# Performance work log

Hardware: AMD Instinct MI355X
Metric: run time of the kernel (lower is better)

Reference implementation:

```python
import jax, jax.numpy as jnp
import numpy as np

N_NODES = 50000
N_EDGES = 800000
IN_FEAT = 128
NUM_CLASSES = 40


def _glorot(key, shape):
    fan_in, fan_out = shape
    lim = jnp.sqrt(6.0 / (fan_in + fan_out))
    return jax.random.uniform(key, shape, jnp.float32, -lim, lim)


def setup_inputs() -> dict:
    key = jax.random.key(0)
    ks = jax.random.split(key, 16)
    inp = {
        "x": jax.random.normal(ks[0], (N_NODES, IN_FEAT), jnp.float32),
        "edge_index": jax.random.randint(ks[1], (2, N_EDGES), 0, N_NODES, jnp.int64),
        "edge_weight": jax.random.uniform(ks[2], (N_EDGES,), jnp.float32),
        # GCNConv weights (PyG GCNConv: linear w/o bias, separate bias added after aggregation)
        "W1": _glorot(ks[3], (IN_FEAT, 512)), "b1": jnp.zeros((512,), jnp.float32),
        "W2": _glorot(ks[4], (512, 256)), "b2": jnp.zeros((256,), jnp.float32),
        "W3": _glorot(ks[5], (256, 128)), "b3": jnp.zeros((128,), jnp.float32),
        # MLP head
        "L1w": _glorot(ks[6], (128, 64)), "L1b": jnp.zeros((64,), jnp.float32),
        "L2w": _glorot(ks[7], (64, 32)), "L2b": jnp.zeros((32,), jnp.float32),
        "L3w": _glorot(ks[8], (32, NUM_CLASSES)), "L3b": jnp.zeros((NUM_CLASSES,), jnp.float32),
    }
    return inp


def _gcn_conv(x, W, b, src, dst, ew, n):
    # PyG GCNConv: add self-loops (weight 1), symmetric normalization D^-1/2 (A+I) D^-1/2,
    # linear transform first, then scatter-add aggregation, then bias.
    xw = x @ W  # [N, C_out]
    deg = jax.ops.segment_sum(ew, dst, num_segments=n) + 1.0  # +1 for self-loop weight
    dinv = jnp.where(deg > 0, jax.lax.rsqrt(deg), 0.0)  # [N]
    norm = dinv[src] * ew * dinv[dst]  # [E]
    out = jax.ops.segment_sum(norm[:, None] * xw[src], dst, num_segments=n)
    out = out + (dinv * dinv)[:, None] * xw  # self-loop contribution
    return out + b


def reference(x, edge_index, edge_weight, W1, b1, W2, b2, W3, b3,
              L1w, L1b, L2w, L2b, L3w, L3b):
    n = x.shape[0]
    src, dst = edge_index[0], edge_index[1]
    # conv stack; dropout p=0.0 -> identity (omitted)
    h = jax.nn.relu(_gcn_conv(x, W1, b1, src, dst, edge_weight, n))
    h = jax.nn.relu(_gcn_conv(h, W2, b2, src, dst, edge_weight, n))
    h = jax.nn.relu(_gcn_conv(h, W3, b3, src, dst, edge_weight, n))
    # MLP head
    h = jax.nn.relu(h @ L1w + L1b)
    h = jax.nn.relu(h @ L2w + L2b)
    h = h @ L3w + L3b
    return jax.nn.softmax(h, axis=1)
```

## Files before the change

### kernel.cpp

```cpp
#include <hip/hip_runtime.h>
#include <hip/hip_bf16.h>

#define N_NODES 50000
#define N_EDGES 800000
#define M_PAD 50048

typedef __attribute__((ext_vector_type(8))) short short8;
typedef __attribute__((ext_vector_type(4))) float float4_;

#define GLOAD_LDS(g, l) __builtin_amdgcn_global_load_lds( \
    (const __attribute__((address_space(1))) void*)(g),   \
    (__attribute__((address_space(3))) void*)(l), 16, 0, 0)

__device__ __forceinline__ unsigned short f2bf(float f) {
    unsigned int u = __float_as_uint(f);
    unsigned int r = (u + 0x7FFFu + ((u >> 16) & 1u)) >> 16;
    return (unsigned short)r;
}
__device__ __forceinline__ float bf2f(unsigned short h) {
    return __uint_as_float(((unsigned int)h) << 16);
}


__global__ __launch_bounds__(256) void deg_kernel(const int* __restrict__ dst,
                                                  const float* __restrict__ ew,
                                                  float* __restrict__ deg, int E) {
    int e = blockIdx.x * blockDim.x + threadIdx.x;
    if (e < E) atomicAdd(&deg[dst[e]], ew[e]);
}

__global__ __launch_bounds__(256) void dinv_kernel(float* __restrict__ deg, int n) {
    int i = blockIdx.x * blockDim.x + threadIdx.x;
    if (i < n) deg[i] = rsqrtf(deg[i] + 1.0f);
}


__global__ __launch_bounds__(256) void count_kernel(const int* __restrict__ dst,
                                                    int* __restrict__ cnt, int E) {
    int e = blockIdx.x * blockDim.x + threadIdx.x;
    if (e < E) atomicAdd(&cnt[dst[e]], 1);
}

__global__ __launch_bounds__(512) void scan_block_kernel(const int* __restrict__ cnt,
                                                         int* __restrict__ rowptr,
                                                         int* __restrict__ bsums, int n) {
    __shared__ int s[512];
    int t = threadIdx.x;
    int i = blockIdx.x * 512 + t;
    s[t] = (i < n) ? cnt[i] : 0;
    __syncthreads();
    for (int off = 1; off < 512; off <<= 1) {
        int v = (t >= off) ? s[t - off] : 0;
        __syncthreads();
        s[t] += v;
        __syncthreads();
    }
    if (i < n) rowptr[i + 1] = s[t];
    if (t == 511) bsums[blockIdx.x] = s[511];
}

__global__ void scan_sums_kernel(int* bsums, int nb) {
    if (threadIdx.x == 0 && blockIdx.x == 0) {
        int run = 0;
        for (int i = 0; i < nb; ++i) { int v = bsums[i]; bsums[i] = run; run += v; }
    }
}

__global__ __launch_bounds__(512) void scan_add_kernel(int* __restrict__ rowptr,
                                                       const int* __restrict__ bsums, int n) {
    int i = blockIdx.x * 512 + threadIdx.x;
    if (i < n) rowptr[i + 1] += bsums[blockIdx.x];
    if (i == 0) rowptr[0] = 0;
}

__global__ __launch_bounds__(256) void fill_kernel(const int* __restrict__ src,
                                                   const int* __restrict__ dst,
                                                   const float* __restrict__ ew,
                                                   const float* __restrict__ dinv,
                                                   int* __restrict__ cursor,
                                                   int* __restrict__ col,
                                                   float* __restrict__ val, int E) {
    int e = blockIdx.x * blockDim.x + threadIdx.x;
    if (e >= E) return;
    int d = dst[e];
    int s = src[e];
    int pos = atomicAdd(&cursor[d], 1);
    col[pos] = s;
    val[pos] = dinv[s] * ew[e];
}


__global__ __launch_bounds__(256) void wsplit_kernel(const float* __restrict__ Wm,
                                                     unsigned short* __restrict__ Th,
                                                     unsigned short* __restrict__ Tl,
                                                     int K, int N) {
    int idx = blockIdx.x * blockDim.x + threadIdx.x;
    if (idx >= K * N) return;
    int n = idx / K, k = idx - n * K;
    float v = Wm[(size_t)k * N + n];
    unsigned short hi = f2bf(v);
    float res = v - bf2f(hi);
    Th[idx] = hi;
    Tl[idx] = f2bf(res);
}


template <int C, bool BIAS, bool RELU, bool SPLIT>
__global__ __launch_bounds__(256) void gather_kernel(const float* __restrict__ t,
                                                     const int* __restrict__ rowptr,
                                                     const int* __restrict__ col,
                                                     const float* __restrict__ val,
                                                     const float* __restrict__ dinv,
                                                     const float* __restrict__ bias,
                                                     float* __restrict__ outf,
                                                     unsigned short* __restrict__ oh,
                                                     unsigned short* __restrict__ ol, int n) {
    constexpr int R = C / 64;
    int wave = threadIdx.x >> 6, lane = threadIdx.x & 63;
    for (int node = blockIdx.x * 4 + wave; node < n; node += gridDim.x * 4) {
        float acc[R];
#pragma unroll
        for (int r = 0; r < R; ++r) acc[r] = 0.f;
        int p0 = rowptr[node], p1 = rowptr[node + 1];
        for (int p = p0; p < p1; ++p) {
            int s = col[p];
            float a = val[p];
            const float* tr = t + (size_t)s * C;
#pragma unroll
            for (int r = 0; r < R; ++r) acc[r] += a * tr[r * 64 + lane];
        }
        float di = dinv[node];
        const float* tn = t + (size_t)node * C;
#pragma unroll
        for (int r = 0; r < R; ++r) {
            float v = di * acc[r] + di * di * tn[r * 64 + lane];
            if (BIAS) v += bias[r * 64 + lane];
            if (RELU) v = fmaxf(v, 0.f);
            size_t idx = (size_t)node * C + r * 64 + lane;
            if (SPLIT) {
                unsigned short hi = f2bf(v);
                float res = v - bf2f(hi);
                oh[idx] = hi;
                ol[idx] = f2bf(res);
            } else {
                outf[idx] = v;
            }
        }
    }
}


template <int OUTMODE>
__global__ __launch_bounds__(256, 2) void mfma_gemm(const unsigned short* __restrict__ Ah,
                                                    const unsigned short* __restrict__ Al,
                                                    const unsigned short* __restrict__ Bh,
                                                    const unsigned short* __restrict__ Bl,
                                                    const float* __restrict__ bias,
                                                    float* __restrict__ Cf,
                                                    unsigned short* __restrict__ Ch,
                                                    unsigned short* __restrict__ Cl,
                                                    int K, int N) {
    __shared__ unsigned short sAh[128 * 64];
    __shared__ unsigned short sAl[128 * 64];
    __shared__ unsigned short sBh[128 * 64];
    __shared__ unsigned short sBl[128 * 64];

    int tid = threadIdx.x;
    int lane = tid & 63, w = tid >> 6;
    int m0 = blockIdx.x * 128, n0 = blockIdx.y * 128;

    const unsigned short* gsrc = (w == 0) ? Ah : (w == 1) ? Al : (w == 2) ? Bh : Bl;
    unsigned short* sbase = (w == 0) ? sAh : (w == 1) ? sAl : (w == 2) ? sBh : sBl;
    int grow0 = ((w < 2) ? m0 : n0) + (lane >> 3);
    int gcol = ((lane & 7) ^ ((lane >> 3) & 7)) * 8;
    const unsigned short* gptr0 = gsrc + (size_t)grow0 * K + gcol;

    float4_ acc[4][4] = {};

    int wm = (w >> 1) * 64, wn = (w & 1) * 64;
    int lr = lane & 15, lg = lane >> 4;

    for (int k0 = 0; k0 < K; k0 += 64) {
        const unsigned short* gp = gptr0 + k0;
#pragma unroll
        for (int q = 0; q < 16; ++q)
            GLOAD_LDS(gp + (size_t)(8 * q) * K, sbase + q * 512);
        __syncthreads();

#pragma unroll
        for (int ks = 0; ks < 2; ++ks) {
            short8 ahf[4], alf[4], bhf[4], blf[4];
#pragma unroll
            for (int f = 0; f < 4; ++f) {
                int ra = wm + f * 16 + lr;
                int sa = (((ks << 2) | lg) ^ (ra & 7)) * 16;
                ahf[f] = *(const short8*)((const char*)sAh + ra * 128 + sa);
                alf[f] = *(const short8*)((const char*)sAl + ra * 128 + sa);
                int rb = wn + f * 16 + lr;
                int sb = (((ks << 2) | lg) ^ (rb & 7)) * 16;
                bhf[f] = *(const short8*)((const char*)sBh + rb * 128 + sb);
                blf[f] = *(const short8*)((const char*)sBl + rb * 128 + sb);
            }
#pragma unroll
            for (int i = 0; i < 4; ++i)
#pragma unroll
                for (int j = 0; j < 4; ++j) {
                    acc[i][j] = __builtin_amdgcn_mfma_f32_16x16x32_bf16(ahf[i], bhf[j], acc[i][j], 0, 0, 0);
                    acc[i][j] = __builtin_amdgcn_mfma_f32_16x16x32_bf16(ahf[i], blf[j], acc[i][j], 0, 0, 0);
                    acc[i][j] = __builtin_amdgcn_mfma_f32_16x16x32_bf16(alf[i], bhf[j], acc[i][j], 0, 0, 0);
                }
        }
        __syncthreads();
    }

#pragma unroll
    for (int i = 0; i < 4; ++i) {
        int row0 = m0 + wm + i * 16 + lg * 4;
#pragma unroll
        for (int j = 0; j < 4; ++j) {
            int colg = n0 + wn + j * 16 + lr;
            float b = (OUTMODE == 1) ? bias[colg] : 0.f;
#pragma unroll
            for (int r = 0; r < 4; ++r) {
                float v = acc[i][j][r] + b;
                size_t idx = (size_t)(row0 + r) * N + colg;
                if (OUTMODE == 1) {
                    v = fmaxf(v, 0.f);
                    unsigned short hi = f2bf(v);
                    float res = v - bf2f(hi);
                    Ch[idx] = hi;
                    Cl[idx] = f2bf(res);
                } else {
                    Cf[idx] = v;
                }
            }
        }
    }
}


__global__ __launch_bounds__(256) void mlp_kernel(const float* __restrict__ h,
                                                  const float* __restrict__ W1, const float* __restrict__ b1,
                                                  const float* __restrict__ W2, const float* __restrict__ b2,
                                                  const float* __restrict__ W3, const float* __restrict__ b3,
                                                  float* __restrict__ out, int n) {
    __shared__ float W1s[128 * 64];
    __shared__ float W2s[64 * 32];
    __shared__ float W3s[32 * 40];
    __shared__ float b1s[64], b2s[32], b3s[40];
    __shared__ float hs[4][128];
    __shared__ float h1s[4][64];
    __shared__ float h2s[4][32];
    __shared__ float ls[4][40];
    __shared__ float es[4][40];

    int tid = threadIdx.x;
    for (int i = tid; i < 128 * 64; i += 256) W1s[i] = W1[i];
    for (int i = tid; i < 64 * 32; i += 256) W2s[i] = W2[i];
    for (int i = tid; i < 32 * 40; i += 256) W3s[i] = W3[i];
    if (tid < 64) b1s[tid] = b1[tid];
    if (tid < 32) b2s[tid] = b2[tid];
    if (tid < 40) b3s[tid] = b3[tid];
    __syncthreads();

    int wave = tid >> 6, lane = tid & 63;

    for (int base = blockIdx.x * 4; base < n; base += gridDim.x * 4) {
        int node = base + wave;
        if (node < n) {
            hs[wave][lane]      = fmaxf(h[(size_t)node * 128 + lane], 0.f);
            hs[wave][lane + 64] = fmaxf(h[(size_t)node * 128 + lane + 64], 0.f);
        }
        __syncthreads();
        {
            float acc = b1s[lane];
#pragma unroll 8
            for (int k = 0; k < 128; ++k) acc += hs[wave][k] * W1s[k * 64 + lane];
            h1s[wave][lane] = fmaxf(acc, 0.f);
        }
        __syncthreads();
        if (lane < 32) {
            float acc = b2s[lane];
#pragma unroll 8
            for (int k = 0; k < 64; ++k) acc += h1s[wave][k] * W2s[k * 32 + lane];
            h2s[wave][lane] = fmaxf(acc, 0.f);
        }
        __syncthreads();
        if (lane < 40) {
            float acc = b3s[lane];
#pragma unroll 8
            for (int k = 0; k < 32; ++k) acc += h2s[wave][k] * W3s[k * 40 + lane];
            ls[wave][lane] = acc;
        }
        __syncthreads();
        float e = 0.f;
        if (lane < 40) {
            float m = -1e30f;
            for (int j = 0; j < 40; ++j) m = fmaxf(m, ls[wave][j]);
            e = expf(ls[wave][lane] - m);
            es[wave][lane] = e;
        }
        __syncthreads();
        if (node < n && lane < 40) {
            float s = 0.f;
            for (int j = 0; j < 40; ++j) s += es[wave][j];
            out[(size_t)node * 40 + lane] = e / s;
        }
        __syncthreads();
    }
}


extern "C" void kernel_launch(void* const* d_in, const int* in_sizes, int n_in,
                              void* d_out, int out_size, void* d_ws, size_t ws_size,
                              hipStream_t stream) {
    const float* x   = (const float*)d_in[0];
    const int*   ei  = (const int*)d_in[1];
    const float* ew  = (const float*)d_in[2];
    const float* W1  = (const float*)d_in[3];
    const float* b1  = (const float*)d_in[4];
    const float* W2  = (const float*)d_in[5];
    const float* b2  = (const float*)d_in[6];
    const float* W3  = (const float*)d_in[7];
    const float* b3  = (const float*)d_in[8];
    const float* L1w = (const float*)d_in[9];
    const float* L1b = (const float*)d_in[10];
    const float* L2w = (const float*)d_in[11];
    const float* L2b = (const float*)d_in[12];
    const float* L3w = (const float*)d_in[13];
    const float* L3b = (const float*)d_in[14];
    float* out = (float*)d_out;

    const int n = N_NODES, E = N_EDGES;
    const int* src = ei;
    const int* dst = ei + E;

    char* wsb = (char*)d_ws;
    size_t off = 0;
    auto alloc = [&](size_t bytes) -> char* {
        char* p = wsb + off;
        off += (bytes + 255) & ~(size_t)255;
        return p;
    };
    float* dinv   = (float*)alloc(N_NODES * 4);
    int* rowptr   = (int*)alloc((N_NODES + 1) * 4);
    int* cursor   = (int*)alloc(N_NODES * 4);
    int* colb     = (int*)alloc((size_t)N_EDGES * 4);
    float* val    = (float*)alloc((size_t)N_EDGES * 4);
    int* bsums    = (int*)alloc(256 * 4);
    unsigned short* W1th = (unsigned short*)alloc(512 * 128 * 2);
    unsigned short* W1tl = (unsigned short*)alloc(512 * 128 * 2);
    unsigned short* W2th = (unsigned short*)alloc(256 * 512 * 2);
    unsigned short* W2tl = (unsigned short*)alloc(256 * 512 * 2);
    unsigned short* W3th = (unsigned short*)alloc(128 * 256 * 2);
    unsigned short* W3tl = (unsigned short*)alloc(128 * 256 * 2);
    unsigned short* aggXh = (unsigned short*)alloc((size_t)M_PAD * 128 * 2);
    unsigned short* aggXl = (unsigned short*)alloc((size_t)M_PAD * 128 * 2);
    unsigned short* h1h  = (unsigned short*)alloc((size_t)M_PAD * 512 * 2);
    unsigned short* h1l  = (unsigned short*)alloc((size_t)M_PAD * 512 * 2);
    float* t2     = (float*)alloc((size_t)M_PAD * 256 * 4);
    unsigned short* agg2h = aggXh;
    unsigned short* agg2l = (unsigned short*)h1h;
    float* t3   = (float*)((char*)h1h + (size_t)M_PAD * 256 * 2);
    float* agg3 = (float*)h1l;

    const int nb = (n + 511) / 512;

    hipMemsetAsync(dinv, 0, n * sizeof(float), stream);
    deg_kernel<<<(E + 255) / 256, 256, 0, stream>>>(dst, ew, dinv, E);
    dinv_kernel<<<(n + 255) / 256, 256, 0, stream>>>(dinv, n);

    wsplit_kernel<<<(128 * 512 + 255) / 256, 256, 0, stream>>>(W1, W1th, W1tl, 128, 512);
    wsplit_kernel<<<(512 * 256 + 255) / 256, 256, 0, stream>>>(W2, W2th, W2tl, 512, 256);
    wsplit_kernel<<<(256 * 128 + 255) / 256, 256, 0, stream>>>(W3, W3th, W3tl, 256, 128);

    hipMemsetAsync(cursor, 0, n * sizeof(int), stream);
    count_kernel<<<(E + 255) / 256, 256, 0, stream>>>(dst, cursor, E);
    scan_block_kernel<<<nb, 512, 0, stream>>>(cursor, rowptr, bsums, n);
    scan_sums_kernel<<<1, 64, 0, stream>>>(bsums, nb);
    scan_add_kernel<<<nb, 512, 0, stream>>>(rowptr, bsums, n);
    hipMemcpyAsync(cursor, rowptr, n * sizeof(int), hipMemcpyDeviceToDevice, stream);
    fill_kernel<<<(E + 255) / 256, 256, 0, stream>>>(src, dst, ew, dinv, cursor, colb, val, E);

    gather_kernel<128, false, false, true><<<(n + 3) / 4, 256, 0, stream>>>(
        x, rowptr, colb, val, dinv, nullptr, nullptr, aggXh, aggXl, n);
    {
        dim3 g(M_PAD / 128, 512 / 128);
        mfma_gemm<1><<<g, 256, 0, stream>>>(aggXh, aggXl, W1th, W1tl, b1, nullptr, h1h, h1l, 128, 512);
    }
    {
        dim3 g(M_PAD / 128, 256 / 128);
        mfma_gemm<0><<<g, 256, 0, stream>>>(h1h, h1l, W2th, W2tl, nullptr, t2, nullptr, nullptr, 512, 256);
    }
    gather_kernel<256, true, true, true><<<(n + 3) / 4, 256, 0, stream>>>(
        t2, rowptr, colb, val, dinv, b2, nullptr, agg2h, agg2l, n);
    {
        dim3 g(M_PAD / 128, 128 / 128);
        mfma_gemm<0><<<g, 256, 0, stream>>>(agg2h, agg2l, W3th, W3tl, nullptr, t3, nullptr, nullptr, 256, 128);
    }
    gather_kernel<128, true, false, false><<<(n + 3) / 4, 256, 0, stream>>>(
        t3, rowptr, colb, val, dinv, b3, agg3, nullptr, nullptr, n);
    mlp_kernel<<<1024, 256, 0, stream>>>(agg3, L1w, L1b, L2w, L2b, L3w, L3b, out, n);
}
```

Baseline: 761.9 us.

## Vectorize SpMM gather with float4 loads and unrolled multi-edge batching

Reworks the CSR gather kernel so each lane handles four contiguous features through float4 loads. When C is 128 the wave splits into two edge slots that are reduced with a cross-lane shuffle. Edges are processed four at a time per slot, with clamped index loads, so several independent row fetches are in flight to hide gather latency. Epilogue stores are vectorized as float4 or ushort4. The cost is extra masked loads on the tail and, for C=128, half the lanes sit idle during the epilogue.

```diff
diff --git a/kernel.cpp b/kernel.cpp
--- a/kernel.cpp
+++ b/kernel.cpp
@@ -115,35 +115,75 @@
                                                      float* __restrict__ outf,
                                                      unsigned short* __restrict__ oh,
                                                      unsigned short* __restrict__ ol, int n) {
-    constexpr int R = C / 64;
+    constexpr int L = C / 4;
+    constexpr int EPS = 64 / L;
+    constexpr int U = 4;
     int wave = threadIdx.x >> 6, lane = threadIdx.x & 63;
+    int slot = lane / L, li = lane % L;
+
     for (int node = blockIdx.x * 4 + wave; node < n; node += gridDim.x * 4) {
-        float acc[R];
-#pragma unroll
-        for (int r = 0; r < R; ++r) acc[r] = 0.f;
         int p0 = rowptr[node], p1 = rowptr[node + 1];
-        for (int p = p0; p < p1; ++p) {
-            int s = col[p];
-            float a = val[p];
-            const float* tr = t + (size_t)s * C;
-#pragma unroll
-            for (int r = 0; r < R; ++r) acc[r] += a * tr[r * 64 + lane];
-        }
-        float di = dinv[node];
-        const float* tn = t + (size_t)node * C;
-#pragma unroll
-        for (int r = 0; r < R; ++r) {
-            float v = di * acc[r] + di * di * tn[r * 64 + lane];
-            if (BIAS) v += bias[r * 64 + lane];
-            if (RELU) v = fmaxf(v, 0.f);
-            size_t idx = (size_t)node * C + r * 64 + lane;
+        float4 acc = {0.f, 0.f, 0.f, 0.f};
+        for (int pb = p0; pb < p1; pb += U * EPS) {
+            float a[U];
+            float4 v[U];
+#pragma unroll
+            for (int u = 0; u < U; ++u) {
+                int pe = pb + u * EPS + slot;
+                int pec = min(pe, p1 - 1);
+                int s = col[pec];
+                float av = val[pec];
+                a[u] = (pe < p1) ? av : 0.f;
+                v[u] = *(const float4*)(t + (size_t)s * C + li * 4);
+            }
+#pragma unroll
+            for (int u = 0; u < U; ++u) {
+                acc.x += a[u] * v[u].x;
+                acc.y += a[u] * v[u].y;
+                acc.z += a[u] * v[u].z;
+                acc.w += a[u] * v[u].w;
+            }
+        }
+        if (EPS == 2) {
+            acc.x += __shfl_xor(acc.x, 32);
+            acc.y += __shfl_xor(acc.y, 32);
+            acc.z += __shfl_xor(acc.z, 32);
+            acc.w += __shfl_xor(acc.w, 32);
+        }
+        if (EPS == 1 || slot == 0) {
+            float di = dinv[node];
+            float s2 = di * di;
+            float4 tv = *(const float4*)(t + (size_t)node * C + li * 4);
+            float4 r;
+            r.x = di * acc.x + s2 * tv.x;
+            r.y = di * acc.y + s2 * tv.y;
+            r.z = di * acc.z + s2 * tv.z;
+            r.w = di * acc.w + s2 * tv.w;
+            if (BIAS) {
+                float4 b4 = *(const float4*)(bias + li * 4);
+                r.x += b4.x; r.y += b4.y; r.z += b4.z; r.w += b4.w;
+            }
+            if (RELU) {
+                r.x = fmaxf(r.x, 0.f); r.y = fmaxf(r.y, 0.f);
+                r.z = fmaxf(r.z, 0.f); r.w = fmaxf(r.w, 0.f);
+            }
+            size_t base = (size_t)node * C + li * 4;
             if (SPLIT) {
-                unsigned short hi = f2bf(v);
-                float res = v - bf2f(hi);
-                oh[idx] = hi;
-                ol[idx] = f2bf(res);
+                ushort4 h4, l4;
+                float rv[4] = {r.x, r.y, r.z, r.w};
+                unsigned short hs[4], lsx[4];
+#pragma unroll
+                for (int j = 0; j < 4; ++j) {
+                    unsigned short hi = f2bf(rv[j]);
+                    hs[j] = hi;
+                    lsx[j] = f2bf(rv[j] - bf2f(hi));
+                }
+                h4.x = hs[0]; h4.y = hs[1]; h4.z = hs[2]; h4.w = hs[3];
+                l4.x = lsx[0]; l4.y = lsx[1]; l4.z = lsx[2]; l4.w = lsx[3];
+                *(ushort4*)(oh + base) = h4;
+                *(ushort4*)(ol + base) = l4;
             } else {
-                outf[idx] = v;
+                *(float4*)(outf + base) = r;
             }
         }
     }
```

Result: faster. 715.4 us (-6.1%).
